# Performance work log

Hardware: AMD Instinct MI355X
Metric: run time of the kernel (lower is better)

## Reference

```python
import jax, jax.numpy as jnp
import numpy as np

TAU = 2.0      # spikingjelly LIFNode default tau
V_TH = 1.0     # default v_threshold
ALPHA = 4.0    # default surrogate.Sigmoid alpha


@jax.custom_vjp
def spike_fn(v):
    # Heaviside(v - v_th) with sigmoid surrogate gradient
    return (v >= V_TH).astype(v.dtype)

def _spike_fwd(v):
    return (v >= V_TH).astype(v.dtype), v

def _spike_bwd(v, g):
    s = jax.nn.sigmoid(ALPHA * (v - V_TH))
    return (g * ALPHA * s * (1.0 - s),)

spike_fn.defvjp(_spike_fwd, _spike_bwd)


def lif(x):
    """Multi-step LIF: decay_input=False, hard reset to v_reset=0, detach_reset.
    x: [T, B, C, N] -> spikes [T, B, C, N]."""
    def step(v, xt):
        v = v * (1.0 - 1.0 / TAU) + xt          # v = v - (v - 0)/tau + x
        s = spike_fn(v)
        v = v * (1.0 - jax.lax.stop_gradient(s))  # hard reset, detached spike
        return v, s
    v0 = jnp.zeros_like(x[0])
    _, spikes = jax.lax.scan(step, v0, x)
    return spikes


def setup_inputs() -> dict:
    key = jax.random.key(0)
    kx, k1, k2, k3 = jax.random.split(key, 4)
    T, B, C, dim = 4, 32, 196, 768
    scale = dim ** -0.5
    x = jax.random.normal(kx, (T, B, C, dim), dtype=jnp.float32)
    w1 = jax.random.normal(k1, (dim, dim), dtype=jnp.float32) * scale
    w2 = jax.random.normal(k2, (dim, dim), dtype=jnp.float32) * scale
    w3 = jax.random.normal(k3, (dim, dim), dtype=jnp.float32) * scale
    return {"x": x, "w1": w1, "w2": w2, "w3": w3}


def reference(x, w1, w2, w3):
    # y1 = mlp1(mlp1_lif(x)); y2 = mlp2(mlp2_lif(x)); out = mlp3(y1 * mlp3_lif(y2))
    y1 = jnp.einsum('tbcn,mn->tbcm', lif(x), w1)
    y2 = jnp.einsum('tbcn,mn->tbcm', lif(x), w2)
    out = jnp.einsum('tbcn,mn->tbcm', y1 * lif(y2), w3)
    return out
```

## Files before the change

### kernel.cpp

```cpp
#include <hip/hip_runtime.h>
#include <stdint.h>

#define T_STEPS 4
#define BC      6272
#define NDIM    768
#define TBC     (T_STEPS*BC)
#define BCN     (BC*NDIM)
#define FIX_CAP 65536

typedef unsigned short u16;
typedef __attribute__((ext_vector_type(8))) __bf16 bf16x8;
typedef __attribute__((ext_vector_type(4))) float f32x4;
typedef __attribute__((ext_vector_type(4))) int   i32x4;

#define MFMA16(a,b,c)  __builtin_amdgcn_mfma_f32_16x16x32_bf16((a),(b),(c),0,0,0)
#define MFMAI8(a,b,c)  __builtin_amdgcn_mfma_i32_16x16x64_i8((a),(b),(c),0,0,0)

__device__ __forceinline__ u16 f2b(float f) {
    uint32_t u = __builtin_bit_cast(uint32_t, f);
    u += 0x7FFFu + ((u >> 16) & 1u);
    return (u16)(u >> 16);
}
__device__ __forceinline__ void gload16(const void* g, void* l) {
    __builtin_amdgcn_global_load_lds((const __attribute__((address_space(1))) void*)g,
                                     (__attribute__((address_space(3))) void*)l,
                                     16, 0, 0);
}

__global__ __launch_bounds__(256) void front_kernel(
    const float* __restrict__ x,
    const float* __restrict__ w1, const float* __restrict__ w2,
    const float* __restrict__ w3,
    int8_t* __restrict__ s8, u16* __restrict__ cnt,
    int8_t* __restrict__ w1q, int8_t* __restrict__ w2h,
    int8_t* __restrict__ w2l, u16* __restrict__ w3b,
    uint32_t* __restrict__ fix_cnt)
{
    if (blockIdx.x < BC / 4) {
        const int bc   = blockIdx.x * 4 + (threadIdx.x >> 6);
        const int lane = threadIdx.x & 63;
        const size_t base = (size_t)bc * NDIM + lane * 12;

        double v[12];
        #pragma unroll
        for (int j = 0; j < 12; ++j) v[j] = 0.0;
        uint32_t c01 = 0, c23 = 0;

        #pragma unroll
        for (int t = 0; t < T_STEPS; ++t) {
            float4 xa = *(const float4*)&x[(size_t)t * BCN + base + 0];
            float4 xb = *(const float4*)&x[(size_t)t * BCN + base + 4];
            float4 xc = *(const float4*)&x[(size_t)t * BCN + base + 8];
            float xs[12] = {xa.x, xa.y, xa.z, xa.w, xb.x, xb.y, xb.z, xb.w,
                            xc.x, xc.y, xc.z, xc.w};
            uint32_t pk[3] = {0, 0, 0};
            uint32_t csum = 0;
            #pragma unroll
            for (int j = 0; j < 12; ++j) {
                v[j] = 0.5 * v[j] + (double)xs[j];
                if (v[j] >= 1.0) {
                    pk[j >> 2] |= 1u << ((j & 3) * 8);
                    csum++;
                    v[j] = 0.0;
                }
            }
            uint32_t* dst = (uint32_t*)&s8[(size_t)t * BCN + base];
            dst[0] = pk[0]; dst[1] = pk[1]; dst[2] = pk[2];
            if (t < 2) c01 += csum << (t * 16);
            else       c23 += csum << ((t - 2) * 16);
        }
        #pragma unroll
        for (int o = 32; o > 0; o >>= 1) {
            c01 += __shfl_xor(c01, o);
            c23 += __shfl_xor(c23, o);
        }
        if (lane == 0) {
            cnt[0 * BC + bc] = (u16)(c01 & 0xFFFF);
            cnt[1 * BC + bc] = (u16)(c01 >> 16);
            cnt[2 * BC + bc] = (u16)(c23 & 0xFFFF);
            cnt[3 * BC + bc] = (u16)(c23 >> 16);
        }
    } else {
        int i = (blockIdx.x - BC / 4) * 256 + threadIdx.x;
        if (i == 0) *fix_cnt = 0;
        int q1 = __float2int_rn(w1[i] * 512.0f);
        q1 = q1 > 127 ? 127 : (q1 < -127 ? -127 : q1);
        w1q[i] = (int8_t)q1;
        int q16 = __double2int_rn((double)w2[i] * 65536.0);
        int8_t lo = (int8_t)(q16 & 0xFF);
        int hi = (q16 - (int)lo) >> 8;
        w2h[i] = (int8_t)hi;
        w2l[i] = lo;
        w3b[i] = f2b(w3[i]);
    }
}

__global__ __launch_bounds__(256) void y12_kernel(
    const int8_t* __restrict__ s8,
    const int8_t* __restrict__ w1q, const int8_t* __restrict__ w2hb,
    const int8_t* __restrict__ w2lb,
    const u16* __restrict__ cnt,
    u16* __restrict__ z,
    uint32_t* __restrict__ fix_cnt,
    int2* __restrict__ fix_idx, float4* __restrict__ fix_y1)
{
    __shared__ int8_t lds[2][40960];

    const int tid  = threadIdx.x;
    const int lane = tid & 63;
    const int wid  = tid >> 6;

    const int bid = blockIdx.x;
    const int swz = (bid & 7) * 294 + (bid >> 3);
    const int mb  = swz % (NDIM / 64);
    const int rb  = swz / (NDIM / 64);
    const int m0  = mb * 64;
    const int bc0 = rb * 32;

    const int srow  = lane >> 3;
    const int scolB = ((lane & 7) << 4) ^ (srow << 4);
    const int8_t* gp[10];
    int lofs[10];
    #pragma unroll
    for (int c = 0; c < 10; ++c) {
        int chunk = wid * 10 + c;
        const int8_t* g;
        int l;
        if (chunk < 16) {
            int gr = chunk * 8 + srow;
            int t = gr >> 5, bcl = gr & 31;
            g = s8 + ((size_t)(t * BC + bc0 + bcl)) * NDIM + scolB;
            l = chunk * 1024;
        } else if (chunk < 24) {
            int mr = (chunk - 16) * 8 + srow;
            g = w1q + ((size_t)(m0 + mr)) * NDIM + scolB;
            l = 16384 + (chunk - 16) * 1024;
        } else if (chunk < 32) {
            int mr = (chunk - 24) * 8 + srow;
            g = w2hb + ((size_t)(m0 + mr)) * NDIM + scolB;
            l = 24576 + (chunk - 24) * 1024;
        } else {
            int mr = (chunk - 32) * 8 + srow;
            g = w2lb + ((size_t)(m0 + mr)) * NDIM + scolB;
            l = 32768 + (chunk - 32) * 1024;
        }
        gp[c] = g;
        lofs[c] = l;
    }

    const int key = lane & 7;
    const int g4  = lane >> 4;
    int slotA[2];
    slotA[0] = ((g4     ^ key) << 4);
    slotA[1] = (((4|g4) ^ key) << 4);
    int abase[8];
    #pragma unroll
    for (int t = 0; t < 4; ++t)
        #pragma unroll
        for (int rt = 0; rt < 2; ++rt)
            abase[t * 2 + rt] = (t * 32 + rt * 16 + (lane & 15)) * 128;
    const int bbase = (wid * 16 + (lane & 15)) * 128;

    i32x4 acc1[4][2], acch[4][2], accl[4][2];
    #pragma unroll
    for (int t = 0; t < 4; ++t)
        #pragma unroll
        for (int rt = 0; rt < 2; ++rt) {
            acc1[t][rt] = (i32x4){0, 0, 0, 0};
            acch[t][rt] = (i32x4){0, 0, 0, 0};
            accl[t][rt] = (i32x4){0, 0, 0, 0};
        }

    auto stage = [&](int buf) {
        #pragma unroll
        for (int c = 0; c < 10; ++c) {
            gload16(gp[c], &lds[buf][lofs[c]]);
            gp[c] += 128;
        }
    };
    auto compute = [&](int buf) {
        const int8_t* L = lds[buf];
        #pragma unroll
        for (int ks = 0; ks < 2; ++ks) {
            const int sl = slotA[ks];
            i32x4 b1 = *(const i32x4*)&L[16384 + bbase + sl];
            i32x4 bh = *(const i32x4*)&L[24576 + bbase + sl];
            i32x4 bl = *(const i32x4*)&L[32768 + bbase + sl];
            #pragma unroll
            for (int t = 0; t < 4; ++t)
                #pragma unroll
                for (int rt = 0; rt < 2; ++rt) {
                    i32x4 a = *(const i32x4*)&L[abase[t * 2 + rt] + sl];
                    acc1[t][rt] = MFMAI8(a, b1, acc1[t][rt]);
                    acch[t][rt] = MFMAI8(a, bh, acch[t][rt]);
                    accl[t][rt] = MFMAI8(a, bl, accl[t][rt]);
                }
        }
    };

    stage(0);
    __syncthreads();
    #pragma unroll
    for (int it = 0; it < 5; ++it) {
        stage((it + 1) & 1);
        compute(it & 1);
        __syncthreads();
    }
    compute(1);

    const int mg = m0 + wid * 16 + (lane & 15);
    #pragma unroll
    for (int rt = 0; rt < 2; ++rt) {
        #pragma unroll
        for (int r = 0; r < 4; ++r) {
            const int bcg = bc0 + rt * 16 + (lane >> 4) * 4 + r;
            double v = 0.0, e = 0.0;
            bool flag = false;
            float zv[4], y1v[4];
            #pragma unroll
            for (int t = 0; t < 4; ++t) {
                float y1 = (float)acc1[t][rt][r] * (1.0f / 512.0f);
                y1v[t] = y1;
                double y2 = (double)(acch[t][rt][r] * 256 + accl[t][rt][r])
                            * (1.0 / 65536.0);
                v = 0.5 * v + y2;
                e = 0.5 * e + 7.62939453125e-6 * (double)cnt[t * BC + bcg] + 1e-9;
                double d = v - 1.0;
                flag |= (d <= e && d >= -e);
                if (v >= 1.0) { zv[t] = y1; v = 0.0; e = 0.0; }
                else          { zv[t] = 0.0f; }
            }
            if (flag) {
                uint32_t id = atomicAdd(fix_cnt, 1u);
                if (id < FIX_CAP) {
                    fix_idx[id] = make_int2(bcg, mg);
                    fix_y1[id]  = make_float4(y1v[0], y1v[1], y1v[2], y1v[3]);
                }
            }
            #pragma unroll
            for (int t = 0; t < 4; ++t)
                z[((size_t)(t * BC + bcg)) * NDIM + mg] = f2b(zv[t]);
        }
    }
}

__global__ __launch_bounds__(256) void fixup_kernel(
    const int8_t* __restrict__ s8, const float* __restrict__ w2,
    const int2* __restrict__ fix_idx, const float4* __restrict__ fix_y1,
    const uint32_t* __restrict__ fix_cnt, u16* __restrict__ z)
{
    const int lane = threadIdx.x & 63;
    const int wave = (blockIdx.x * 256 + threadIdx.x) >> 6;
    const int nw   = gridDim.x * 4;
    uint32_t n = *fix_cnt;
    if (n > FIX_CAP) n = FIX_CAP;

    for (uint32_t e = wave; e < n; e += nw) {
        const int bc = fix_idx[e].x, m = fix_idx[e].y;
        const float* w2row = w2 + (size_t)m * NDIM;
        double acc[4] = {0.0, 0.0, 0.0, 0.0};
        #pragma unroll
        for (int j = 0; j < NDIM / 64; ++j) {
            int nn = lane + j * 64;
            double wv = (double)w2row[nn];
            #pragma unroll
            for (int t = 0; t < 4; ++t)
                if (s8[((size_t)(t * BC + bc)) * NDIM + nn]) acc[t] += wv;
        }
        #pragma unroll
        for (int o = 32; o > 0; o >>= 1)
            #pragma unroll
            for (int t = 0; t < 4; ++t) acc[t] += __shfl_xor(acc[t], o);
        if (lane == 0) {
            float4 y1 = fix_y1[e];
            float y1a[4] = {y1.x, y1.y, y1.z, y1.w};
            double v = 0.0;
            #pragma unroll
            for (int t = 0; t < 4; ++t) {
                v = 0.5 * v + acc[t];
                u16 zz = 0;
                if (v >= 1.0) { zz = f2b(y1a[t]); v = 0.0; }
                z[((size_t)(t * BC + bc)) * NDIM + m] = zz;
            }
        }
    }
}

__global__ __launch_bounds__(256, 2) void out_kernel(
    const u16* __restrict__ z, const u16* __restrict__ w3b,
    float* __restrict__ out)
{
    __shared__ u16 lds[2][16384];

    const int lane = threadIdx.x & 63;
    const int wid  = threadIdx.x >> 6;
    const int rw   = wid >> 1;
    const int cw   = wid & 1;

    const int bid = blockIdx.x;
    const int swz = (bid & 7) * 147 + (bid >> 3);
    const int mb  = swz % (NDIM / 128);
    const int rb  = swz / (NDIM / 128);
    const int m0  = mb * 128;
    const int r0  = rb * 128;

    const int srow  = lane >> 3;
    const int scolE = ((((lane & 7) << 4) ^ ((srow & 7) << 4)) >> 1);
    const u16* gp[8];
    int lofs[8];
    #pragma unroll
    for (int c = 0; c < 8; ++c) {
        int chunk = wid * 8 + c;
        const u16* g;
        if (chunk < 16) {
            int gr = chunk * 8 + srow;
            g = z + ((size_t)(r0 + gr)) * NDIM + scolE;
        } else {
            int mr = (chunk - 16) * 8 + srow;
            g = w3b + ((size_t)(m0 + mr)) * NDIM + scolE;
        }
        gp[c] = g;
        lofs[c] = chunk * 512;
    }

    const int swzb = (lane & 7) << 4;
    const int cb   = (lane >> 4) << 4;
    const int colE0 = ((cb     ) ^ swzb) >> 1;
    const int colE1 = ((cb | 64) ^ swzb) >> 1;

    f32x4 acc[4][4];
    #pragma unroll
    for (int rt = 0; rt < 4; ++rt)
        #pragma unroll
        for (int cf = 0; cf < 4; ++cf) acc[rt][cf] = (f32x4){0.f, 0.f, 0.f, 0.f};

    auto stage = [&](int buf) {
        #pragma unroll
        for (int c = 0; c < 8; ++c) {
            gload16(gp[c], &lds[buf][lofs[c]]);
            gp[c] += 64;
        }
    };
    auto compute = [&](int buf) {
        const u16* L = lds[buf];
        #pragma unroll
        for (int k2i = 0; k2i < 2; ++k2i) {
            const int ce = k2i ? colE1 : colE0;
            bf16x8 bw[4];
            #pragma unroll
            for (int cf = 0; cf < 4; ++cf)
                bw[cf] = *(const bf16x8*)&L[8192 + (cw * 64 + cf * 16 + (lane & 15)) * 64 + ce];
            #pragma unroll
            for (int rt = 0; rt < 4; ++rt) {
                bf16x8 az = *(const bf16x8*)&L[(rw * 64 + rt * 16 + (lane & 15)) * 64 + ce];
                #pragma unroll
                for (int cf = 0; cf < 4; ++cf)
                    acc[rt][cf] = MFMA16(az, bw[cf], acc[rt][cf]);
            }
        }
    };

    stage(0);
    __syncthreads();
    for (int it = 0; it < 11; ++it) {
        stage((it + 1) & 1);
        compute(it & 1);
        __syncthreads();
    }
    compute(1);

    #pragma unroll
    for (int rt = 0; rt < 4; ++rt)
        #pragma unroll
        for (int cf = 0; cf < 4; ++cf)
            #pragma unroll
            for (int r = 0; r < 4; ++r)
                out[((size_t)(r0 + rw * 64 + rt * 16 + (lane >> 4) * 4 + r)) * NDIM
                    + m0 + cw * 64 + cf * 16 + (lane & 15)] = acc[rt][cf][r];
}

extern "C" void kernel_launch(void* const* d_in, const int* in_sizes, int n_in,
                              void* d_out, int out_size, void* d_ws, size_t ws_size,
                              hipStream_t stream) {
    const float* x  = (const float*)d_in[0];
    const float* w1 = (const float*)d_in[1];
    const float* w2 = (const float*)d_in[2];
    const float* w3 = (const float*)d_in[3];
    float* out = (float*)d_out;

    char* ws = (char*)d_ws;
    int8_t*   s8      = (int8_t*)(ws);
    u16*      z       = (u16*)(ws + 19267584);
    int8_t*   w1q     = (int8_t*)(ws + 57802752);
    int8_t*   w2h     = (int8_t*)(ws + 58392576);
    int8_t*   w2l     = (int8_t*)(ws + 58982400);
    u16*      w3b     = (u16*)(ws + 59572224);
    u16*      cnt     = (u16*)(ws + 60751872);
    uint32_t* fix_cnt = (uint32_t*)(ws + 60802048);
    int2*     fix_idx = (int2*)(ws + 60802112);
    float4*   fix_y1  = (float4*)(ws + 61326400);

    front_kernel<<<BC / 4 + (NDIM * NDIM) / 256, 256, 0, stream>>>(
        x, w1, w2, w3, s8, cnt, w1q, w2h, w2l, w3b, fix_cnt);
    y12_kernel<<<(BC / 32) * (NDIM / 64), 256, 0, stream>>>(s8, w1q, w2h, w2l,
                                                            cnt, z, fix_cnt,
                                                            fix_idx, fix_y1);
    fixup_kernel<<<512, 256, 0, stream>>>(s8, w2, fix_idx, fix_y1, fix_cnt, z);
    out_kernel<<<(TBC / 128) * (NDIM / 128), 256, 0, stream>>>(z, w3b, out);
}
```

Before: 120.8 us.

## Replace dense output GEMM with spike-mask sparse row accumulation

The y12 and fixup kernels now record, for each output row, a bitmask of which mlp3_lif spikes fired; z is written only at those positions. The dense bf16 MFMA out_kernel is replaced by a per-row kernel that walks the mask and accumulates the matching rows of a transposed bf16 w3 with scalar FMAs. The aim is to skip the zero entries of the third matmul. The cost is atomicOr traffic, a data-dependent serial loop per wave, and scalar FP32 math instead of matrix cores, so the gain depends heavily on how sparse the spikes are.

```diff
diff --git a/kernel.cpp b/kernel.cpp
--- a/kernel.cpp
+++ b/kernel.cpp
@@ -7,19 +7,23 @@
 #define TBC     (T_STEPS*BC)
 #define BCN     (BC*NDIM)
 #define FIX_CAP 65536
+#define MASKW   (TBC * 24)
 
 typedef unsigned short u16;
 typedef __attribute__((ext_vector_type(8))) __bf16 bf16x8;
 typedef __attribute__((ext_vector_type(4))) float f32x4;
 typedef __attribute__((ext_vector_type(4))) int   i32x4;
 
-#define MFMA16(a,b,c)  __builtin_amdgcn_mfma_f32_16x16x32_bf16((a),(b),(c),0,0,0)
 #define MFMAI8(a,b,c)  __builtin_amdgcn_mfma_i32_16x16x64_i8((a),(b),(c),0,0,0)
 
 __device__ __forceinline__ u16 f2b(float f) {
     uint32_t u = __builtin_bit_cast(uint32_t, f);
     u += 0x7FFFu + ((u >> 16) & 1u);
     return (u16)(u >> 16);
+}
+__device__ __forceinline__ float b2f(u16 b) {
+    uint32_t u = ((uint32_t)b) << 16;
+    return __builtin_bit_cast(float, u);
 }
 __device__ __forceinline__ void gload16(const void* g, void* l) {
     __builtin_amdgcn_global_load_lds((const __attribute__((address_space(1))) void*)g,
@@ -33,8 +37,8 @@
     const float* __restrict__ w3,
     int8_t* __restrict__ s8, u16* __restrict__ cnt,
     int8_t* __restrict__ w1q, int8_t* __restrict__ w2h,
-    int8_t* __restrict__ w2l, u16* __restrict__ w3b,
-    uint32_t* __restrict__ fix_cnt)
+    int8_t* __restrict__ w2l, u16* __restrict__ w3T,
+    uint32_t* __restrict__ rowmask, uint32_t* __restrict__ fix_cnt)
 {
     if (blockIdx.x < BC / 4) {
         const int bc   = blockIdx.x * 4 + (threadIdx.x >> 6);
@@ -91,7 +95,9 @@
         int hi = (q16 - (int)lo) >> 8;
         w2h[i] = (int8_t)hi;
         w2l[i] = lo;
-        w3b[i] = f2b(w3[i]);
+        w3T[i] = f2b(w3[(size_t)(i % NDIM) * NDIM + (i / NDIM)]);
+        rowmask[i] = 0;
+        if (i < MASKW - NDIM * NDIM) rowmask[NDIM * NDIM + i] = 0;
     }
 }
 
@@ -100,7 +106,7 @@
     const int8_t* __restrict__ w1q, const int8_t* __restrict__ w2hb,
     const int8_t* __restrict__ w2lb,
     const u16* __restrict__ cnt,
-    u16* __restrict__ z,
+    u16* __restrict__ z, uint32_t* __restrict__ rowmask,
     uint32_t* __restrict__ fix_cnt,
     int2* __restrict__ fix_idx, float4* __restrict__ fix_y1)
 {
@@ -216,6 +222,7 @@
             const int bcg = bc0 + rt * 16 + (lane >> 4) * 4 + r;
             double v = 0.0, e = 0.0;
             bool flag = false;
+            int sp = 0;
             float zv[4], y1v[4];
             #pragma unroll
             for (int t = 0; t < 4; ++t) {
@@ -227,7 +234,7 @@
                 e = 0.5 * e + 7.62939453125e-6 * (double)cnt[t * BC + bcg] + 1e-9;
                 double d = v - 1.0;
                 flag |= (d <= e && d >= -e);
-                if (v >= 1.0) { zv[t] = y1; v = 0.0; e = 0.0; }
+                if (v >= 1.0) { zv[t] = y1; sp |= 1 << t; v = 0.0; e = 0.0; }
                 else          { zv[t] = 0.0f; }
             }
             if (flag) {
@@ -236,10 +243,16 @@
                     fix_idx[id] = make_int2(bcg, mg);
                     fix_y1[id]  = make_float4(y1v[0], y1v[1], y1v[2], y1v[3]);
                 }
+            } else if (sp) {
+                #pragma unroll
+                for (int t = 0; t < 4; ++t)
+                    if ((sp >> t) & 1) {
+                        int row = t * BC + bcg;
+                        z[(size_t)row * NDIM + mg] = f2b(zv[t]);
+                        atomicOr(&rowmask[(size_t)row * 24 + (mg >> 5)],
+                                 1u << (mg & 31));
+                    }
             }
-            #pragma unroll
-            for (int t = 0; t < 4; ++t)
-                z[((size_t)(t * BC + bcg)) * NDIM + mg] = f2b(zv[t]);
         }
     }
 }
@@ -247,7 +260,8 @@
 __global__ __launch_bounds__(256) void fixup_kernel(
     const int8_t* __restrict__ s8, const float* __restrict__ w2,
     const int2* __restrict__ fix_idx, const float4* __restrict__ fix_y1,
-    const uint32_t* __restrict__ fix_cnt, u16* __restrict__ z)
+    const uint32_t* __restrict__ fix_cnt,
+    u16* __restrict__ z, uint32_t* __restrict__ rowmask)
 {
     const int lane = threadIdx.x & 63;
     const int wave = (blockIdx.x * 256 + threadIdx.x) >> 6;
@@ -278,105 +292,55 @@
             #pragma unroll
             for (int t = 0; t < 4; ++t) {
                 v = 0.5 * v + acc[t];
-                u16 zz = 0;
-                if (v >= 1.0) { zz = f2b(y1a[t]); v = 0.0; }
-                z[((size_t)(t * BC + bc)) * NDIM + m] = zz;
+                if (v >= 1.0) {
+                    int row = t * BC + bc;
+                    z[(size_t)row * NDIM + m] = f2b(y1a[t]);
+                    atomicOr(&rowmask[(size_t)row * 24 + (m >> 5)],
+                             1u << (m & 31));
+                    v = 0.0;
+                }
             }
         }
     }
 }
 
-__global__ __launch_bounds__(256, 2) void out_kernel(
-    const u16* __restrict__ z, const u16* __restrict__ w3b,
-    float* __restrict__ out)
+__global__ __launch_bounds__(256) void out_sparse_kernel(
+    const u16* __restrict__ z, const u16* __restrict__ w3T,
+    const uint32_t* __restrict__ rowmask, float* __restrict__ out)
 {
-    __shared__ u16 lds[2][16384];
-
+    const int r    = blockIdx.x * 4 + (threadIdx.x >> 6);
     const int lane = threadIdx.x & 63;
-    const int wid  = threadIdx.x >> 6;
-    const int rw   = wid >> 1;
-    const int cw   = wid & 1;
-
-    const int bid = blockIdx.x;
-    const int swz = (bid & 7) * 147 + (bid >> 3);
-    const int mb  = swz % (NDIM / 128);
-    const int rb  = swz / (NDIM / 128);
-    const int m0  = mb * 128;
-    const int r0  = rb * 128;
-
-    const int srow  = lane >> 3;
-    const int scolE = ((((lane & 7) << 4) ^ ((srow & 7) << 4)) >> 1);
-    const u16* gp[8];
-    int lofs[8];
-    #pragma unroll
-    for (int c = 0; c < 8; ++c) {
-        int chunk = wid * 8 + c;
-        const u16* g;
-        if (chunk < 16) {
-            int gr = chunk * 8 + srow;
-            g = z + ((size_t)(r0 + gr)) * NDIM + scolE;
-        } else {
-            int mr = (chunk - 16) * 8 + srow;
-            g = w3b + ((size_t)(m0 + mr)) * NDIM + scolE;
-        }
-        gp[c] = g;
-        lofs[c] = chunk * 512;
-    }
-
-    const int swzb = (lane & 7) << 4;
-    const int cb   = (lane >> 4) << 4;
-    const int colE0 = ((cb     ) ^ swzb) >> 1;
-    const int colE1 = ((cb | 64) ^ swzb) >> 1;
-
-    f32x4 acc[4][4];
-    #pragma unroll
-    for (int rt = 0; rt < 4; ++rt)
-        #pragma unroll
-        for (int cf = 0; cf < 4; ++cf) acc[rt][cf] = (f32x4){0.f, 0.f, 0.f, 0.f};
-
-    auto stage = [&](int buf) {
-        #pragma unroll
-        for (int c = 0; c < 8; ++c) {
-            gload16(gp[c], &lds[buf][lofs[c]]);
-            gp[c] += 64;
-        }
-    };
-    auto compute = [&](int buf) {
-        const u16* L = lds[buf];
-        #pragma unroll
-        for (int k2i = 0; k2i < 2; ++k2i) {
-            const int ce = k2i ? colE1 : colE0;
-            bf16x8 bw[4];
-            #pragma unroll
-            for (int cf = 0; cf < 4; ++cf)
-                bw[cf] = *(const bf16x8*)&L[8192 + (cw * 64 + cf * 16 + (lane & 15)) * 64 + ce];
-            #pragma unroll
-            for (int rt = 0; rt < 4; ++rt) {
-                bf16x8 az = *(const bf16x8*)&L[(rw * 64 + rt * 16 + (lane & 15)) * 64 + ce];
-                #pragma unroll
-                for (int cf = 0; cf < 4; ++cf)
-                    acc[rt][cf] = MFMA16(az, bw[cf], acc[rt][cf]);
-            }
-        }
-    };
-
-    stage(0);
-    __syncthreads();
-    for (int it = 0; it < 11; ++it) {
-        stage((it + 1) & 1);
-        compute(it & 1);
-        __syncthreads();
-    }
-    compute(1);
-
-    #pragma unroll
-    for (int rt = 0; rt < 4; ++rt)
-        #pragma unroll
-        for (int cf = 0; cf < 4; ++cf)
-            #pragma unroll
-            for (int r = 0; r < 4; ++r)
-                out[((size_t)(r0 + rw * 64 + rt * 16 + (lane >> 4) * 4 + r)) * NDIM
-                    + m0 + cw * 64 + cf * 16 + (lane & 15)] = acc[rt][cf][r];
+    const int base = lane * 4;
+
+    f32x4 a0 = {0.f, 0.f, 0.f, 0.f};
+    f32x4 a1 = {0.f, 0.f, 0.f, 0.f};
+    f32x4 a2 = {0.f, 0.f, 0.f, 0.f};
+
+    const uint32_t* mw = rowmask + (size_t)r * 24;
+    #pragma unroll 4
+    for (int w = 0; w < 24; ++w) {
+        uint32_t bits = mw[w];
+        while (bits) {
+            int b = __ffs(bits) - 1;
+            bits &= bits - 1;
+            int m = w * 32 + b;
+            float val = b2f(z[(size_t)r * NDIM + m]);
+            const u16* wr = &w3T[(size_t)m * NDIM + base];
+            ushort4 q0 = *(const ushort4*)&wr[0];
+            ushort4 q1 = *(const ushort4*)&wr[256];
+            ushort4 q2 = *(const ushort4*)&wr[512];
+            a0[0] += val * b2f(q0.x); a0[1] += val * b2f(q0.y);
+            a0[2] += val * b2f(q0.z); a0[3] += val * b2f(q0.w);
+            a1[0] += val * b2f(q1.x); a1[1] += val * b2f(q1.y);
+            a1[2] += val * b2f(q1.z); a1[3] += val * b2f(q1.w);
+            a2[0] += val * b2f(q2.x); a2[1] += val * b2f(q2.y);
+            a2[2] += val * b2f(q2.z); a2[3] += val * b2f(q2.w);
+        }
+    }
+    float* orow = out + (size_t)r * NDIM + base;
+    *(f32x4*)&orow[0]   = a0;
+    *(f32x4*)&orow[256] = a1;
+    *(f32x4*)&orow[512] = a2;
 }
 
 extern "C" void kernel_launch(void* const* d_in, const int* in_sizes, int n_in,
@@ -394,17 +358,18 @@
     int8_t*   w1q     = (int8_t*)(ws + 57802752);
     int8_t*   w2h     = (int8_t*)(ws + 58392576);
     int8_t*   w2l     = (int8_t*)(ws + 58982400);
-    u16*      w3b     = (u16*)(ws + 59572224);
+    u16*      w3T     = (u16*)(ws + 59572224);
     u16*      cnt     = (u16*)(ws + 60751872);
     uint32_t* fix_cnt = (uint32_t*)(ws + 60802048);
     int2*     fix_idx = (int2*)(ws + 60802112);
     float4*   fix_y1  = (float4*)(ws + 61326400);
+    uint32_t* rowmask = (uint32_t*)(ws + 62374976);
 
     front_kernel<<<BC / 4 + (NDIM * NDIM) / 256, 256, 0, stream>>>(
-        x, w1, w2, w3, s8, cnt, w1q, w2h, w2l, w3b, fix_cnt);
-    y12_kernel<<<(BC / 32) * (NDIM / 64), 256, 0, stream>>>(s8, w1q, w2h, w2l,
-                                                            cnt, z, fix_cnt,
-                                                            fix_idx, fix_y1);
-    fixup_kernel<<<512, 256, 0, stream>>>(s8, w2, fix_idx, fix_y1, fix_cnt, z);
-    out_kernel<<<(TBC / 128) * (NDIM / 128), 256, 0, stream>>>(z, w3b, out);
-}
+        x, w1, w2, w3, s8, cnt, w1q, w2h, w2l, w3T, rowmask, fix_cnt);
+    y12_kernel<<<(BC / 32) * (NDIM / 64), 256, 0, stream>>>(
+        s8, w1q, w2h, w2l, cnt, z, rowmask, fix_cnt, fix_idx, fix_y1);
+    fixup_kernel<<<512, 256, 0, stream>>>(s8, w2, fix_idx, fix_y1, fix_cnt,
+                                          z, rowmask);
+    out_sparse_kernel<<<TBC / 4, 256, 0, stream>>>(z, w3T, rowmask, out);
+}
```

After: 156.5 us. 29.5% more time.
